# Kernel tuning notes

Measured on AMD Instinct MI355X. Metric: run time of the kernel, lower is better.

## Reference

```python
import jax, jax.numpy as jnp
import numpy as np

N_HEAD = 16
N_EMBD = 1024
HEAD_DIM = N_EMBD // N_HEAD
ROPE_BASE = 10000.0


def _rope_tables(T, dim):
    inv_freq = 1.0 / (ROPE_BASE ** (jnp.arange(0, dim, 2, dtype=jnp.float32) / dim))
    t = jnp.arange(T, dtype=jnp.float32)
    freqs = jnp.einsum('i,j->ij', t, inv_freq)          # [T, dim/2]
    emb = jnp.concatenate((freqs, freqs), axis=-1)       # [T, dim]
    return jnp.cos(emb), jnp.sin(emb)


def _rotate_half(x):
    x1, x2 = jnp.split(x, 2, axis=-1)
    return jnp.concatenate((-x2, x1), axis=-1)


def setup_inputs() -> dict:
    key = jax.random.key(0)
    k_x, k_wa, k_ba, k_wp, k_bp = jax.random.split(key, 5)
    B, T, C = 2, 2048, N_EMBD
    x = jax.random.normal(k_x, (B, T, C), dtype=jnp.float32)
    # torch Linear weights: [out, in]
    W_attn = jax.random.normal(k_wa, (3 * C, C), dtype=jnp.float32) * (1.0 / np.sqrt(C))
    b_attn = jax.random.normal(k_ba, (3 * C,), dtype=jnp.float32) * 0.01
    W_proj = jax.random.normal(k_wp, (C, C), dtype=jnp.float32) * (1.0 / np.sqrt(C))
    b_proj = jax.random.normal(k_bp, (C,), dtype=jnp.float32) * 0.01
    return {"x": x, "W_attn": W_attn, "b_attn": b_attn, "W_proj": W_proj, "b_proj": b_proj}


def reference(x, W_attn, b_attn, W_proj, b_proj):
    B, T, C = x.shape
    H, D = N_HEAD, HEAD_DIM
    qkv = jnp.einsum('btc,oc->bto', x, W_attn) + b_attn   # [B,T,3C]
    q, k, v = jnp.split(qkv, 3, axis=2)
    # [B,T,C] -> [B,H,T,D]
    q = q.reshape(B, T, H, D).transpose(0, 2, 1, 3)
    k = k.reshape(B, T, H, D).transpose(0, 2, 1, 3)
    v = v.reshape(B, T, H, D).transpose(0, 2, 1, 3)
    cos, sin = _rope_tables(T, D)                          # [T,D]
    q = q * cos + _rotate_half(q) * sin
    k = k * cos + _rotate_half(k) * sin
    att = jnp.einsum('bhqd,bhkd->bhqk', q, k) * (1.0 / np.sqrt(D))
    causal = jnp.tril(jnp.ones((T, T), dtype=bool))
    att = jnp.where(causal, att, -jnp.inf)
    att = jax.nn.softmax(att, axis=-1)
    y = jnp.einsum('bhqk,bhkd->bhqd', att, v)              # [B,H,T,D]
    y = y.transpose(0, 2, 1, 3).reshape(B, T, C)
    y = jnp.einsum('btc,oc->bto', y, W_proj) + b_proj
    return y
```

## Files before the change

kernel.cpp:

```cpp
#include <hip/hip_runtime.h>


typedef unsigned short u16;
typedef u16 u16x4 __attribute__((ext_vector_type(4)));
typedef u16 u16x8 __attribute__((ext_vector_type(8)));
typedef short s16x4 __attribute__((ext_vector_type(4)));
typedef short s16x8 __attribute__((ext_vector_type(8)));
typedef float f32x4 __attribute__((ext_vector_type(4)));

#define T_SEQ 2048
#define C_EMB 1024
#define NH 16
#define HD 64

#define MFMA16(a, b, c) __builtin_amdgcn_mfma_f32_16x16x32_bf16(a, b, c, 0, 0, 0)

__device__ __forceinline__ f32x4 MFMA16K16(s16x4 a, s16x4 b, f32x4 c) {
#if __has_builtin(__builtin_amdgcn_mfma_f32_16x16x16bf16_1k)
    return __builtin_amdgcn_mfma_f32_16x16x16bf16_1k(a, b, c, 0, 0, 0);
#else
    asm("v_mfma_f32_16x16x16_bf16 %0, %1, %2, %0" : "+v"(c) : "v"(a), "v"(b));
    return c;
#endif
}

__device__ __forceinline__ u16 f2bf(float f) {
    union { float f; unsigned int i; } x; x.f = f;
    unsigned int r = x.i + 0x7fffu + ((x.i >> 16) & 1u);
    return (u16)(r >> 16);
}
__device__ __forceinline__ u16x4 pack4(f32x4 v) {
    u16x4 o;
#pragma unroll
    for (int j = 0; j < 4; ++j) o[j] = f2bf(v[j]);
    return o;
}
__device__ __forceinline__ s16x4 pack4cvt_s(f32x4 v) {
    union { s16x4 h; unsigned int w[2]; } u;
    asm("v_cvt_pk_bf16_f32 %0, %1, %2" : "=v"(u.w[0]) : "v"(v[0]), "v"(v[1]));
    asm("v_cvt_pk_bf16_f32 %0, %1, %2" : "=v"(u.w[1]) : "v"(v[2]), "v"(v[3]));
    return u.h;
}
__device__ __forceinline__ void gload16(const void* g, void* l) {
    __builtin_amdgcn_global_load_lds(
        (const __attribute__((address_space(1))) unsigned int*)g,
        (__attribute__((address_space(3))) unsigned int*)l, 16, 0, 0);
}

__global__ __launch_bounds__(256) void prep_k(const float* __restrict__ x, const float* __restrict__ Wa,
                                              const float* __restrict__ Wp,
                                              u16* __restrict__ xb, u16* __restrict__ Wab,
                                              u16* __restrict__ Wpb, float2* __restrict__ tab) {
    int bid = blockIdx.x, tid = threadIdx.x;
    if (bid < 4096) {
        const float* src;
        u16* dst;
        int i;
        if (bid < 2048)      { src = x;  dst = xb;  i = bid * 256 + tid; }
        else if (bid < 3584) { src = Wa; dst = Wab; i = (bid - 2048) * 256 + tid; }
        else                 { src = Wp; dst = Wpb; i = (bid - 3584) * 256 + tid; }
        f32x4 a = ((const f32x4*)src)[i * 2];
        f32x4 b = ((const f32x4*)src)[i * 2 + 1];
        u16x8 o;
#pragma unroll
        for (int j = 0; j < 4; ++j) o[j] = f2bf(a[j]);
#pragma unroll
        for (int j = 0; j < 4; ++j) o[4 + j] = f2bf(b[j]);
        ((u16x8*)dst)[i] = o;
    } else {
        int idx = (bid - 4096) * 256 + tid;
        int t = idx >> 5, j = idx & 31;
        float inv = __builtin_exp2f(-0.41524101186092f * (float)j);
        float s_, c_;
        sincosf((float)t * inv, &s_, &c_);
        tab[idx] = make_float2(c_, s_);
    }
}

__global__ __launch_bounds__(256) void qkv_rope_k(const u16* __restrict__ xb, const u16* __restrict__ Wab,
                                                  const float* __restrict__ bias,
                                                  const float2* __restrict__ tab,
                                                  u16* __restrict__ qb, u16* __restrict__ kb,
                                                  u16* __restrict__ vt) {
    __shared__ u16 smem[17408];
    u16* As = smem;
    u16* Bs = smem + 8192;
    int tid = threadIdx.x;
    int n0 = blockIdx.x * 128, m0 = blockIdx.y * 128;
    int w = tid >> 6, lane = tid & 63, lr = lane & 15, quad = lane >> 4;
    int wr = w >> 1, wc = w & 1;
    f32x4 acc[4][4] = {};
    int srow = tid >> 2;
    int swc8 = (((tid & 3) ^ (srow & 3)) << 3);
    int soff = tid * 8;
    int rc8 = ((quad ^ (lr & 3)) << 3);

#define QKV_STAGE(bufi, kc) do {                                                   \
        int _b = (bufi) * 4096;                                                    \
        gload16(xb  + (size_t)(m0 + srow) * C_EMB + (kc) + swc8,      &As[_b + soff]);        \
        gload16(xb  + (size_t)(m0 + 64 + srow) * C_EMB + (kc) + swc8, &As[_b + 2048 + soff]); \
        gload16(Wab + (size_t)(n0 + srow) * C_EMB + (kc) + swc8,      &Bs[_b + soff]);        \
        gload16(Wab + (size_t)(n0 + 64 + srow) * C_EMB + (kc) + swc8, &Bs[_b + 2048 + soff]); \
    } while (0)

    QKV_STAGE(0, 0);
#pragma unroll 2
    for (int kt = 0; kt < 32; ++kt) {
        int cur = kt & 1;
        if (kt < 31) {
            QKV_STAGE(cur ^ 1, (kt + 1) * 32);
            asm volatile("s_waitcnt vmcnt(4)" ::: "memory");
        } else {
            asm volatile("s_waitcnt vmcnt(0)" ::: "memory");
        }
        __builtin_amdgcn_s_barrier();
        asm volatile("" ::: "memory");
        int cb = cur * 4096;
        s16x8 af[4], bf[4];
#pragma unroll
        for (int i = 0; i < 4; ++i)
            af[i] = *(const s16x8*)&As[cb + (wr * 64 + i * 16 + lr) * 32 + rc8];
#pragma unroll
        for (int j = 0; j < 4; ++j)
            bf[j] = *(const s16x8*)&Bs[cb + (wc * 64 + j * 16 + lr) * 32 + rc8];
#pragma unroll
        for (int i = 0; i < 4; ++i)
#pragma unroll
            for (int j = 0; j < 4; ++j) acc[i][j] = MFMA16(af[i], bf[j], acc[i][j]);
        asm volatile("" ::: "memory");
        __builtin_amdgcn_s_barrier();
    }
#undef QKV_STAGE

    int sec = n0 >> 10;
    float bv[4];
#pragma unroll
    for (int j = 0; j < 4; ++j) bv[j] = bias[n0 + wc * 64 + j * 16 + lr];

    int h0 = (n0 & 1023) >> 6;
    int b = m0 >> 11, tbase = m0 & 2047;
    if (sec == 2) {
        u16* Ct = smem;
#pragma unroll
        for (int i = 0; i < 4; ++i)
#pragma unroll
            for (int j = 0; j < 4; ++j) {
                f32x4 vv;
#pragma unroll
                for (int r = 0; r < 4; ++r) vv[r] = acc[i][j][r] + bv[j];
                int d = wc * 64 + j * 16 + lr;
                int m4 = wr * 64 + i * 16 + quad * 4;
                *(u16x4*)&Ct[d * 136 + m4] = pack4(vv);
            }
        __syncthreads();
        size_t hb = (size_t)(b * NH);
#pragma unroll
        for (int p = 0; p < 8; ++p) {
            int idx = p * 256 + tid;
            int d = idx >> 4, mc = (idx & 15) << 3;
            s16x8 vdat = *(const s16x8*)&Ct[d * 136 + mc];
            int h = h0 + (d >> 6), dd = d & 63;
            *(s16x8*)(vt + ((hb + h) * HD + dd) * T_SEQ + tbase + mc) = vdat;
        }
    } else {
        u16* dst = (sec == 0) ? qb : kb;
        float qs = (sec == 0) ? 0.18033688011112043f : 1.0f;
        u16* Ct = smem;
        __syncthreads();
#pragma unroll
        for (int i = 0; i < 4; ++i)
#pragma unroll
            for (int r = 0; r < 4; ++r) {
                int mrow = wr * 64 + i * 16 + quad * 4 + r;
                int t = (m0 + mrow) & 2047;
#pragma unroll
                for (int j = 0; j < 2; ++j) {
                    int d1 = j * 16 + lr;
                    float2 cs = tab[t * 32 + d1];
                    float v1 = acc[i][j][r] + bv[j];
                    float v2 = acc[i][j + 2][r] + bv[j + 2];
                    int n1 = wc * 64 + j * 16 + lr;
                    Ct[mrow * 136 + n1]      = f2bf((v1 * cs.x - v2 * cs.y) * qs);
                    Ct[mrow * 136 + n1 + 32] = f2bf((v2 * cs.x + v1 * cs.y) * qs);
                }
            }
        __syncthreads();
#pragma unroll
        for (int p = 0; p < 8; ++p) {
            int idx = p * 256 + tid;
            int mrow = idx >> 4, c = idx & 15;
            s16x8 vdat = *(const s16x8*)&Ct[mrow * 136 + c * 8];
            int h = h0 + (c >> 3), dd = (c & 7) << 3;
            *(s16x8*)(dst + ((size_t)(b * NH + h) * T_SEQ + tbase + mrow) * HD + dd) = vdat;
        }
    }
}

__global__ __launch_bounds__(512, 4) void flash_k(const u16* __restrict__ qb, const u16* __restrict__ kb,
                                                  const u16* __restrict__ vt, u16* __restrict__ yab) {
    __shared__ u16 Ks[2][64 * 72];
    __shared__ u16 Vs[2][64 * 72];
    int tid = threadIdx.x;
    int bx = blockIdx.x, by = blockIdx.y;
    int qt = (by < 16) ? (15 - bx) : bx;
    int bh = by;
    int w = tid >> 6, lane = tid & 63, lr = lane & 15, quad = lane >> 4;
    int q0 = qt * 128;
    const u16* qh = qb + (size_t)bh * T_SEQ * HD;
    const u16* kh = kb + (size_t)bh * T_SEQ * HD;
    const u16* vh = vt + (size_t)bh * HD * T_SEQ;

    int rbase = q0 + w * 16;

    s16x8 aq[2];
#pragma unroll
    for (int ks = 0; ks < 2; ++ks)
        aq[ks] = *(const s16x8*)(qh + (size_t)(rbase + lr) * HD + ks * 32 + quad * 8);

    int srow = tid >> 3, sc8 = (tid & 7) << 3;

    float m_i = -1e30f;
    f32x4 l4 = {0.f, 0.f, 0.f, 0.f};
    f32x4 oacc[4] = {};

    int ktmax = 2 * qt + 1;
    {
        s16x8 kr0 = *(const s16x8*)(kh + (size_t)srow * HD + sc8);
        s16x8 vr0 = *(const s16x8*)(vh + (size_t)srow * T_SEQ + sc8);
        *(s16x8*)&Ks[0][srow * 72 + sc8] = kr0;
        *(s16x8*)&Vs[0][srow * 72 + sc8] = vr0;
    }
    __syncthreads();

    for (int kt = 0; kt <= ktmax; ++kt) {
        int cur = kt & 1;
        int k0 = kt * 64;
        bool pf = kt < ktmax;
        s16x8 kr0, vr0;
        if (pf) {
            int kn = k0 + 64;
            kr0 = *(const s16x8*)(kh + (size_t)(kn + srow) * HD + sc8);
            vr0 = *(const s16x8*)(vh + (size_t)srow * T_SEQ + kn + sc8);
        }
        const u16* Kc = Ks[cur];
        const u16* Vc = Vs[cur];

        if (k0 <= rbase + 15) {
            s16x8 ak[2][4];
#pragma unroll
            for (int ks = 0; ks < 2; ++ks)
#pragma unroll
                for (int tc = 0; tc < 4; ++tc)
                    ak[ks][tc] = *(const s16x8*)&Kc[(tc * 16 + lr) * 72 + ks * 32 + quad * 8];
            f32x4 sacc[4] = {};
#pragma unroll
            for (int ks = 0; ks < 2; ++ks)
#pragma unroll
                for (int tc = 0; tc < 4; ++tc) sacc[tc] = MFMA16(ak[ks][tc], aq[ks], sacc[tc]);
            if (k0 + 63 > rbase) {
#pragma unroll
                for (int tc = 0; tc < 4; ++tc)
#pragma unroll
                    for (int r = 0; r < 4; ++r)
                        if (k0 + tc * 16 + quad * 4 + r > rbase + lr) sacc[tc][r] = -1e30f;
            }
            f32x4 mv = sacc[0];
#pragma unroll
            for (int tc = 1; tc < 4; ++tc)
#pragma unroll
                for (int r = 0; r < 4; ++r) mv[r] = fmaxf(mv[r], sacc[tc][r]);
            float loc = fmaxf(fmaxf(mv[0], mv[1]), fmaxf(mv[2], mv[3]));
            bool need = !__all(loc <= m_i + 8.0f);
            float alpha = 1.0f;
            if (need) {
                float mx = fmaxf(loc, __shfl_xor(loc, 16, 64));
                mx = fmaxf(mx, __shfl_xor(mx, 32, 64));
                float mn = fmaxf(m_i, mx);
                alpha = __builtin_exp2f(m_i - mn);
                m_i = mn;
#pragma unroll
                for (int r = 0; r < 4; ++r) l4[r] *= alpha;
            }
            float mnow = m_i;
#pragma unroll
            for (int tc = 0; tc < 4; ++tc)
#pragma unroll
                for (int r = 0; r < 4; ++r) {
                    float p = __builtin_exp2f(sacc[tc][r] - mnow);
                    sacc[tc][r] = p;
                    l4[r] += p;
                }
            s16x4 pa[4];
#pragma unroll
            for (int tc = 0; tc < 4; ++tc) pa[tc] = pack4cvt_s(sacc[tc]);
            if (need) {
#pragma unroll
                for (int dn = 0; dn < 4; ++dn)
#pragma unroll
                    for (int r = 0; r < 4; ++r) oacc[dn][r] *= alpha;
            }
#pragma unroll
            for (int dn = 0; dn < 4; ++dn) {
                const u16* vrow = &Vc[(dn * 16 + lr) * 72 + quad * 4];
#pragma unroll
                for (int tc = 0; tc < 4; ++tc) {
                    s16x4 vv = *(const s16x4*)(vrow + tc * 16);
                    oacc[dn] = MFMA16K16(vv, pa[tc], oacc[dn]);
                }
            }
        }
        if (pf) {
            int nx = cur ^ 1;
            *(s16x8*)&Ks[nx][srow * 72 + sc8] = kr0;
            *(s16x8*)&Vs[nx][srow * 72 + sc8] = vr0;
        }
        __syncthreads();
    }
    float rs = (l4[0] + l4[1]) + (l4[2] + l4[3]);
    rs += __shfl_xor(rs, 16, 64);
    rs += __shfl_xor(rs, 32, 64);
    int b = bh >> 4, hh = bh & 15;
    {
        float inv = 1.f / rs;
        int t = rbase + lr;
        size_t base = ((size_t)b * T_SEQ + t) * C_EMB + hh * HD;
#pragma unroll
        for (int dn = 0; dn < 4; ++dn) {
            f32x4 vv;
#pragma unroll
            for (int r = 0; r < 4; ++r) vv[r] = oacc[dn][r] * inv;
            *(u16x4*)(yab + base + dn * 16 + quad * 4) = pack4(vv);
        }
    }
}

__global__ __launch_bounds__(256) void proj_k(const u16* __restrict__ ya, const u16* __restrict__ Wpb,
                                              const float* __restrict__ bias, float* __restrict__ out) {
    __shared__ u16 As[2][2048];
    __shared__ u16 Bs[2][2048];
    int tid = threadIdx.x;
    int n0 = blockIdx.x * 64, m0 = blockIdx.y * 64;
    int w = tid >> 6, lane = tid & 63, lr = lane & 15, quad = lane >> 4;
    int wr = w >> 1, wc = w & 1;
    f32x4 acc[2][2] = {};
    int srow = tid >> 2;
    int swc8 = (((tid & 3) ^ (srow & 3)) << 3);
    int soff = tid * 8;
    int rc8 = ((quad ^ (lr & 3)) << 3);

#define PRJ_STAGE(bufi, kc) do {                                                   \
        gload16(ya  + (size_t)(m0 + srow) * C_EMB + (kc) + swc8, &As[bufi][soff]); \
        gload16(Wpb + (size_t)(n0 + srow) * C_EMB + (kc) + swc8, &Bs[bufi][soff]); \
    } while (0)

    PRJ_STAGE(0, 0);
#pragma unroll 2
    for (int kt = 0; kt < 32; ++kt) {
        int cur = kt & 1;
        if (kt < 31) {
            PRJ_STAGE(cur ^ 1, (kt + 1) * 32);
            asm volatile("s_waitcnt vmcnt(2)" ::: "memory");
        } else {
            asm volatile("s_waitcnt vmcnt(0)" ::: "memory");
        }
        __builtin_amdgcn_s_barrier();
        asm volatile("" ::: "memory");
        s16x8 af[2], bf[2];
#pragma unroll
        for (int i = 0; i < 2; ++i)
            af[i] = *(const s16x8*)&As[cur][(wr * 32 + i * 16 + lr) * 32 + rc8];
#pragma unroll
        for (int j = 0; j < 2; ++j)
            bf[j] = *(const s16x8*)&Bs[cur][(wc * 32 + j * 16 + lr) * 32 + rc8];
#pragma unroll
        for (int i = 0; i < 2; ++i)
#pragma unroll
            for (int j = 0; j < 2; ++j) acc[i][j] = MFMA16(af[i], bf[j], acc[i][j]);
        asm volatile("" ::: "memory");
        __builtin_amdgcn_s_barrier();
    }
#undef PRJ_STAGE

    float bv[2];
#pragma unroll
    for (int j = 0; j < 2; ++j) bv[j] = bias[n0 + wc * 32 + j * 16 + lr];
#pragma unroll
    for (int i = 0; i < 2; ++i)
#pragma unroll
        for (int r = 0; r < 4; ++r) {
            int m = m0 + wr * 32 + i * 16 + quad * 4 + r;
#pragma unroll
            for (int j = 0; j < 2; ++j)
                out[(size_t)m * C_EMB + n0 + wc * 32 + j * 16 + lr] = acc[i][j][r] + bv[j];
        }
}

extern "C" void kernel_launch(void* const* d_in, const int* in_sizes, int n_in,
                              void* d_out, int out_size, void* d_ws, size_t ws_size,
                              hipStream_t stream) {
    const float *x = nullptr, *Wa = nullptr, *ba = nullptr, *Wp = nullptr, *bp = nullptr;
    for (int i = 0; i < n_in; ++i) {
        switch (in_sizes[i]) {
            case 4194304: x  = (const float*)d_in[i]; break;
            case 3145728: Wa = (const float*)d_in[i]; break;
            case 3072:    ba = (const float*)d_in[i]; break;
            case 1048576: Wp = (const float*)d_in[i]; break;
            case 1024:    bp = (const float*)d_in[i]; break;
            default: break;
        }
    }
    float* out = (float*)d_out;

    char* ws = (char*)d_ws;
    u16* qb     = (u16*)(ws);
    u16* kb     = (u16*)(ws + 8388608);
    u16* vt     = (u16*)(ws + 16777216);
    u16* yab    = (u16*)(ws + 25165824);
    float2* tab = (float2*)(ws + 33554432);
    u16* xb     = (u16*)(ws + 35651584);
    u16* Wab    = (u16*)(ws + 44040192);
    u16* Wpb    = (u16*)(ws + 50331648);

    prep_k<<<4352, 256, 0, stream>>>(x, Wa, Wp, xb, Wab, Wpb, tab);
    qkv_rope_k<<<dim3(24, 32), 256, 0, stream>>>(xb, Wab, ba, tab, qb, kb, vt);
    flash_k<<<dim3(16, 32), 512, 0, stream>>>(qb, kb, vt, yab);
    proj_k<<<dim3(16, 64), 256, 0, stream>>>(yab, Wpb, bp, out);
}
```

Before: 195.0 us.

## Process two query strips per wave in flash attention to reuse K/V fragments

The flash kernel now runs with 256 threads (4 waves), and each wave handles two 16-row query strips. The strips are paired so that strip w goes with strip 7-w, which balances causal work across waves. K and V fragments are read from shared memory once per tile and used for both strips, which halves LDS traffic per unit of work and evens out the causal load within a block. The cost is more registers per thread (two sets of accumulators and softmax state) and fewer waves per block, which could reduce latency hiding.

```diff
diff --git a/kernel.cpp b/kernel.cpp
--- a/kernel.cpp
+++ b/kernel.cpp
@@ -196,7 +196,7 @@
     }
 }
 
-__global__ __launch_bounds__(512, 4) void flash_k(const u16* __restrict__ qb, const u16* __restrict__ kb,
+__global__ __launch_bounds__(256, 2) void flash_k(const u16* __restrict__ qb, const u16* __restrict__ kb,
                                                   const u16* __restrict__ vt, u16* __restrict__ yab) {
     __shared__ u16 Ks[2][64 * 72];
     __shared__ u16 Vs[2][64 * 72];
@@ -210,25 +210,33 @@
     const u16* kh = kb + (size_t)bh * T_SEQ * HD;
     const u16* vh = vt + (size_t)bh * HD * T_SEQ;
 
-    int rbase = q0 + w * 16;
-
-    s16x8 aq[2];
-#pragma unroll
-    for (int ks = 0; ks < 2; ++ks)
-        aq[ks] = *(const s16x8*)(qh + (size_t)(rbase + lr) * HD + ks * 32 + quad * 8);
+    int rb[2];
+    rb[0] = q0 + w * 16;
+    rb[1] = q0 + 112 - w * 16;
+
+    s16x8 aq[2][2];
+#pragma unroll
+    for (int s = 0; s < 2; ++s)
+#pragma unroll
+        for (int ks = 0; ks < 2; ++ks)
+            aq[s][ks] = *(const s16x8*)(qh + (size_t)(rb[s] + lr) * HD + ks * 32 + quad * 8);
 
     int srow = tid >> 3, sc8 = (tid & 7) << 3;
 
-    float m_i = -1e30f;
-    f32x4 l4 = {0.f, 0.f, 0.f, 0.f};
-    f32x4 oacc[4] = {};
+    float m_i[2] = {-1e30f, -1e30f};
+    f32x4 l4[2] = {{0.f, 0.f, 0.f, 0.f}, {0.f, 0.f, 0.f, 0.f}};
+    f32x4 oacc[2][4] = {};
 
     int ktmax = 2 * qt + 1;
     {
-        s16x8 kr0 = *(const s16x8*)(kh + (size_t)srow * HD + sc8);
-        s16x8 vr0 = *(const s16x8*)(vh + (size_t)srow * T_SEQ + sc8);
-        *(s16x8*)&Ks[0][srow * 72 + sc8] = kr0;
-        *(s16x8*)&Vs[0][srow * 72 + sc8] = vr0;
+        s16x8 ka = *(const s16x8*)(kh + (size_t)srow * HD + sc8);
+        s16x8 kb2 = *(const s16x8*)(kh + (size_t)(srow + 32) * HD + sc8);
+        s16x8 va = *(const s16x8*)(vh + (size_t)srow * T_SEQ + sc8);
+        s16x8 vb = *(const s16x8*)(vh + (size_t)(srow + 32) * T_SEQ + sc8);
+        *(s16x8*)&Ks[0][srow * 72 + sc8] = ka;
+        *(s16x8*)&Ks[0][(srow + 32) * 72 + sc8] = kb2;
+        *(s16x8*)&Vs[0][srow * 72 + sc8] = va;
+        *(s16x8*)&Vs[0][(srow + 32) * 72 + sc8] = vb;
     }
     __syncthreads();
 
@@ -236,99 +244,113 @@
         int cur = kt & 1;
         int k0 = kt * 64;
         bool pf = kt < ktmax;
-        s16x8 kr0, vr0;
+        s16x8 kr0, kr1, vr0, vr1;
         if (pf) {
             int kn = k0 + 64;
             kr0 = *(const s16x8*)(kh + (size_t)(kn + srow) * HD + sc8);
+            kr1 = *(const s16x8*)(kh + (size_t)(kn + srow + 32) * HD + sc8);
             vr0 = *(const s16x8*)(vh + (size_t)srow * T_SEQ + kn + sc8);
+            vr1 = *(const s16x8*)(vh + (size_t)(srow + 32) * T_SEQ + kn + sc8);
         }
         const u16* Kc = Ks[cur];
         const u16* Vc = Vs[cur];
 
-        if (k0 <= rbase + 15) {
+        if (k0 <= rb[1] + 15) {
             s16x8 ak[2][4];
 #pragma unroll
             for (int ks = 0; ks < 2; ++ks)
 #pragma unroll
                 for (int tc = 0; tc < 4; ++tc)
                     ak[ks][tc] = *(const s16x8*)&Kc[(tc * 16 + lr) * 72 + ks * 32 + quad * 8];
-            f32x4 sacc[4] = {};
-#pragma unroll
-            for (int ks = 0; ks < 2; ++ks)
-#pragma unroll
-                for (int tc = 0; tc < 4; ++tc) sacc[tc] = MFMA16(ak[ks][tc], aq[ks], sacc[tc]);
-            if (k0 + 63 > rbase) {
-#pragma unroll
-                for (int tc = 0; tc < 4; ++tc)
-#pragma unroll
-                    for (int r = 0; r < 4; ++r)
-                        if (k0 + tc * 16 + quad * 4 + r > rbase + lr) sacc[tc][r] = -1e30f;
-            }
-            f32x4 mv = sacc[0];
-#pragma unroll
-            for (int tc = 1; tc < 4; ++tc)
-#pragma unroll
-                for (int r = 0; r < 4; ++r) mv[r] = fmaxf(mv[r], sacc[tc][r]);
-            float loc = fmaxf(fmaxf(mv[0], mv[1]), fmaxf(mv[2], mv[3]));
-            bool need = !__all(loc <= m_i + 8.0f);
-            float alpha = 1.0f;
-            if (need) {
-                float mx = fmaxf(loc, __shfl_xor(loc, 16, 64));
-                mx = fmaxf(mx, __shfl_xor(mx, 32, 64));
-                float mn = fmaxf(m_i, mx);
-                alpha = __builtin_exp2f(m_i - mn);
-                m_i = mn;
-#pragma unroll
-                for (int r = 0; r < 4; ++r) l4[r] *= alpha;
-            }
-            float mnow = m_i;
-#pragma unroll
-            for (int tc = 0; tc < 4; ++tc)
-#pragma unroll
-                for (int r = 0; r < 4; ++r) {
-                    float p = __builtin_exp2f(sacc[tc][r] - mnow);
-                    sacc[tc][r] = p;
-                    l4[r] += p;
-                }
-            s16x4 pa[4];
-#pragma unroll
-            for (int tc = 0; tc < 4; ++tc) pa[tc] = pack4cvt_s(sacc[tc]);
-            if (need) {
-#pragma unroll
-                for (int dn = 0; dn < 4; ++dn)
-#pragma unroll
-                    for (int r = 0; r < 4; ++r) oacc[dn][r] *= alpha;
-            }
+            s16x4 av[4][4];
 #pragma unroll
             for (int dn = 0; dn < 4; ++dn) {
                 const u16* vrow = &Vc[(dn * 16 + lr) * 72 + quad * 4];
 #pragma unroll
-                for (int tc = 0; tc < 4; ++tc) {
-                    s16x4 vv = *(const s16x4*)(vrow + tc * 16);
-                    oacc[dn] = MFMA16K16(vv, pa[tc], oacc[dn]);
+                for (int tc = 0; tc < 4; ++tc)
+                    av[dn][tc] = *(const s16x4*)(vrow + tc * 16);
+            }
+#pragma unroll
+            for (int s = 0; s < 2; ++s) {
+                int rbase = rb[s];
+                if (k0 > rbase + 15) continue;
+                f32x4 sacc[4] = {};
+#pragma unroll
+                for (int ks = 0; ks < 2; ++ks)
+#pragma unroll
+                    for (int tc = 0; tc < 4; ++tc) sacc[tc] = MFMA16(ak[ks][tc], aq[s][ks], sacc[tc]);
+                if (k0 + 63 > rbase) {
+#pragma unroll
+                    for (int tc = 0; tc < 4; ++tc)
+#pragma unroll
+                        for (int r = 0; r < 4; ++r)
+                            if (k0 + tc * 16 + quad * 4 + r > rbase + lr) sacc[tc][r] = -1e30f;
                 }
+                f32x4 mv = sacc[0];
+#pragma unroll
+                for (int tc = 1; tc < 4; ++tc)
+#pragma unroll
+                    for (int r = 0; r < 4; ++r) mv[r] = fmaxf(mv[r], sacc[tc][r]);
+                float loc = fmaxf(fmaxf(mv[0], mv[1]), fmaxf(mv[2], mv[3]));
+                bool need = !__all(loc <= m_i[s] + 8.0f);
+                float alpha = 1.0f;
+                if (need) {
+                    float mx = fmaxf(loc, __shfl_xor(loc, 16, 64));
+                    mx = fmaxf(mx, __shfl_xor(mx, 32, 64));
+                    float mn = fmaxf(m_i[s], mx);
+                    alpha = __builtin_exp2f(m_i[s] - mn);
+                    m_i[s] = mn;
+#pragma unroll
+                    for (int r = 0; r < 4; ++r) l4[s][r] *= alpha;
+                }
+                float mnow = m_i[s];
+#pragma unroll
+                for (int tc = 0; tc < 4; ++tc)
+#pragma unroll
+                    for (int r = 0; r < 4; ++r) {
+                        float p = __builtin_exp2f(sacc[tc][r] - mnow);
+                        sacc[tc][r] = p;
+                        l4[s][r] += p;
+                    }
+                s16x4 pa[4];
+#pragma unroll
+                for (int tc = 0; tc < 4; ++tc) pa[tc] = pack4cvt_s(sacc[tc]);
+                if (need) {
+#pragma unroll
+                    for (int dn = 0; dn < 4; ++dn)
+#pragma unroll
+                        for (int r = 0; r < 4; ++r) oacc[s][dn][r] *= alpha;
+                }
+#pragma unroll
+                for (int dn = 0; dn < 4; ++dn)
+#pragma unroll
+                    for (int tc = 0; tc < 4; ++tc)
+                        oacc[s][dn] = MFMA16K16(av[dn][tc], pa[tc], oacc[s][dn]);
             }
         }
         if (pf) {
             int nx = cur ^ 1;
             *(s16x8*)&Ks[nx][srow * 72 + sc8] = kr0;
+            *(s16x8*)&Ks[nx][(srow + 32) * 72 + sc8] = kr1;
             *(s16x8*)&Vs[nx][srow * 72 + sc8] = vr0;
+            *(s16x8*)&Vs[nx][(srow + 32) * 72 + sc8] = vr1;
         }
         __syncthreads();
     }
-    float rs = (l4[0] + l4[1]) + (l4[2] + l4[3]);
-    rs += __shfl_xor(rs, 16, 64);
-    rs += __shfl_xor(rs, 32, 64);
     int b = bh >> 4, hh = bh & 15;
-    {
+#pragma unroll
+    for (int s = 0; s < 2; ++s) {
+        float rs = (l4[s][0] + l4[s][1]) + (l4[s][2] + l4[s][3]);
+        rs += __shfl_xor(rs, 16, 64);
+        rs += __shfl_xor(rs, 32, 64);
         float inv = 1.f / rs;
-        int t = rbase + lr;
+        int t = rb[s] + lr;
         size_t base = ((size_t)b * T_SEQ + t) * C_EMB + hh * HD;
 #pragma unroll
         for (int dn = 0; dn < 4; ++dn) {
             f32x4 vv;
 #pragma unroll
-            for (int r = 0; r < 4; ++r) vv[r] = oacc[dn][r] * inv;
+            for (int r = 0; r < 4; ++r) vv[r] = oacc[s][dn][r] * inv;
             *(u16x4*)(yab + base + dn * 16 + quad * 4) = pack4(vv);
         }
     }
@@ -423,6 +445,6 @@
 
     prep_k<<<4352, 256, 0, stream>>>(x, Wa, Wp, xb, Wab, Wpb, tab);
     qkv_rope_k<<<dim3(24, 32), 256, 0, stream>>>(xb, Wab, ba, tab, qb, kb, vt);
-    flash_k<<<dim3(16, 32), 512, 0, stream>>>(qb, kb, vt, yab);
+    flash_k<<<dim3(16, 32), 256, 0, stream>>>(qb, kb, vt, yab);
     proj_k<<<dim3(16, 64), 256, 0, stream>>>(yab, Wpb, bp, out);
 }
```

Result: slower. 200.3 us (+2.7%).

## Triple-buffer QKV GEMM loads and shrink flash attention tiles to 64 queries

Applied to the files above, without the earlier changes.

The QKV projection GEMM moves from double to triple buffering in shared memory, so global loads are issued two k-steps ahead with adjusted vmcnt waits. The flash attention kernel changes from 512-thread blocks with 128-query tiles to 256-thread blocks with 64-query tiles. This doubles the grid, removes the per-wave skip branch since every wave now needs every key tile up to the diagonal, and applies the causal mask only on the last tile. V fragments are also loaded into registers before the QK MFMAs. The aim is to hide memory latency and improve load balance across the causal triangle, at the cost of more LDS in the GEMM and more register pressure in attention.

```diff
diff --git a/kernel.cpp b/kernel.cpp
--- a/kernel.cpp
+++ b/kernel.cpp
@@ -82,9 +82,9 @@
                                                   const float2* __restrict__ tab,
                                                   u16* __restrict__ qb, u16* __restrict__ kb,
                                                   u16* __restrict__ vt) {
-    __shared__ u16 smem[17408];
+    __shared__ u16 smem[24576];
     u16* As = smem;
-    u16* Bs = smem + 8192;
+    u16* Bs = smem + 12288;
     int tid = threadIdx.x;
     int n0 = blockIdx.x * 128, m0 = blockIdx.y * 128;
     int w = tid >> 6, lane = tid & 63, lr = lane & 15, quad = lane >> 4;
@@ -104,11 +104,14 @@
     } while (0)
 
     QKV_STAGE(0, 0);
-#pragma unroll 2
+    QKV_STAGE(1, 32);
+    int cur = 0;
     for (int kt = 0; kt < 32; ++kt) {
-        int cur = kt & 1;
-        if (kt < 31) {
-            QKV_STAGE(cur ^ 1, (kt + 1) * 32);
+        if (kt < 30) {
+            int nb = cur + 2; if (nb >= 3) nb -= 3;
+            QKV_STAGE(nb, (kt + 2) * 32);
+            asm volatile("s_waitcnt vmcnt(8)" ::: "memory");
+        } else if (kt == 30) {
             asm volatile("s_waitcnt vmcnt(4)" ::: "memory");
         } else {
             asm volatile("s_waitcnt vmcnt(0)" ::: "memory");
@@ -129,6 +132,7 @@
             for (int j = 0; j < 4; ++j) acc[i][j] = MFMA16(af[i], bf[j], acc[i][j]);
         asm volatile("" ::: "memory");
         __builtin_amdgcn_s_barrier();
+        cur = cur + 1; if (cur >= 3) cur -= 3;
     }
 #undef QKV_STAGE
 
@@ -196,16 +200,16 @@
     }
 }
 
-__global__ __launch_bounds__(512, 4) void flash_k(const u16* __restrict__ qb, const u16* __restrict__ kb,
+__global__ __launch_bounds__(256, 4) void flash_k(const u16* __restrict__ qb, const u16* __restrict__ kb,
                                                   const u16* __restrict__ vt, u16* __restrict__ yab) {
     __shared__ u16 Ks[2][64 * 72];
     __shared__ u16 Vs[2][64 * 72];
     int tid = threadIdx.x;
     int bx = blockIdx.x, by = blockIdx.y;
-    int qt = (by < 16) ? (15 - bx) : bx;
+    int qt = (by < 16) ? (31 - bx) : bx;
     int bh = by;
     int w = tid >> 6, lane = tid & 63, lr = lane & 15, quad = lane >> 4;
-    int q0 = qt * 128;
+    int q0 = qt * 64;
     const u16* qh = qb + (size_t)bh * T_SEQ * HD;
     const u16* kh = kb + (size_t)bh * T_SEQ * HD;
     const u16* vh = vt + (size_t)bh * HD * T_SEQ;
@@ -223,12 +227,16 @@
     f32x4 l4 = {0.f, 0.f, 0.f, 0.f};
     f32x4 oacc[4] = {};
 
-    int ktmax = 2 * qt + 1;
+    int ktmax = qt;
     {
-        s16x8 kr0 = *(const s16x8*)(kh + (size_t)srow * HD + sc8);
-        s16x8 vr0 = *(const s16x8*)(vh + (size_t)srow * T_SEQ + sc8);
-        *(s16x8*)&Ks[0][srow * 72 + sc8] = kr0;
-        *(s16x8*)&Vs[0][srow * 72 + sc8] = vr0;
+        s16x8 ka = *(const s16x8*)(kh + (size_t)srow * HD + sc8);
+        s16x8 kb2 = *(const s16x8*)(kh + (size_t)(srow + 32) * HD + sc8);
+        s16x8 va = *(const s16x8*)(vh + (size_t)srow * T_SEQ + sc8);
+        s16x8 vb = *(const s16x8*)(vh + (size_t)(srow + 32) * T_SEQ + sc8);
+        *(s16x8*)&Ks[0][srow * 72 + sc8] = ka;
+        *(s16x8*)&Ks[0][(srow + 32) * 72 + sc8] = kb2;
+        *(s16x8*)&Vs[0][srow * 72 + sc8] = va;
+        *(s16x8*)&Vs[0][(srow + 32) * 72 + sc8] = vb;
     }
     __syncthreads();
 
@@ -236,83 +244,90 @@
         int cur = kt & 1;
         int k0 = kt * 64;
         bool pf = kt < ktmax;
-        s16x8 kr0, vr0;
+        s16x8 kr0, kr1, vr0, vr1;
         if (pf) {
             int kn = k0 + 64;
             kr0 = *(const s16x8*)(kh + (size_t)(kn + srow) * HD + sc8);
+            kr1 = *(const s16x8*)(kh + (size_t)(kn + srow + 32) * HD + sc8);
             vr0 = *(const s16x8*)(vh + (size_t)srow * T_SEQ + kn + sc8);
+            vr1 = *(const s16x8*)(vh + (size_t)(srow + 32) * T_SEQ + kn + sc8);
         }
         const u16* Kc = Ks[cur];
         const u16* Vc = Vs[cur];
 
-        if (k0 <= rbase + 15) {
-            s16x8 ak[2][4];
-#pragma unroll
-            for (int ks = 0; ks < 2; ++ks)
-#pragma unroll
-                for (int tc = 0; tc < 4; ++tc)
-                    ak[ks][tc] = *(const s16x8*)&Kc[(tc * 16 + lr) * 72 + ks * 32 + quad * 8];
-            f32x4 sacc[4] = {};
-#pragma unroll
-            for (int ks = 0; ks < 2; ++ks)
-#pragma unroll
-                for (int tc = 0; tc < 4; ++tc) sacc[tc] = MFMA16(ak[ks][tc], aq[ks], sacc[tc]);
-            if (k0 + 63 > rbase) {
-#pragma unroll
-                for (int tc = 0; tc < 4; ++tc)
-#pragma unroll
-                    for (int r = 0; r < 4; ++r)
-                        if (k0 + tc * 16 + quad * 4 + r > rbase + lr) sacc[tc][r] = -1e30f;
+        s16x8 ak[2][4];
+#pragma unroll
+        for (int ks = 0; ks < 2; ++ks)
+#pragma unroll
+            for (int tc = 0; tc < 4; ++tc)
+                ak[ks][tc] = *(const s16x8*)&Kc[(tc * 16 + lr) * 72 + ks * 32 + quad * 8];
+        s16x4 av[4][4];
+#pragma unroll
+        for (int dn = 0; dn < 4; ++dn) {
+            const u16* vrow = &Vc[(dn * 16 + lr) * 72 + quad * 4];
+#pragma unroll
+            for (int tc = 0; tc < 4; ++tc)
+                av[dn][tc] = *(const s16x4*)(vrow + tc * 16);
+        }
+        f32x4 sacc[4] = {};
+#pragma unroll
+        for (int ks = 0; ks < 2; ++ks)
+#pragma unroll
+            for (int tc = 0; tc < 4; ++tc) sacc[tc] = MFMA16(ak[ks][tc], aq[ks], sacc[tc]);
+        if (kt == ktmax) {
+#pragma unroll
+            for (int tc = 0; tc < 4; ++tc)
+#pragma unroll
+                for (int r = 0; r < 4; ++r)
+                    if (k0 + tc * 16 + quad * 4 + r > rbase + lr) sacc[tc][r] = -1e30f;
+        }
+        f32x4 mv = sacc[0];
+#pragma unroll
+        for (int tc = 1; tc < 4; ++tc)
+#pragma unroll
+            for (int r = 0; r < 4; ++r) mv[r] = fmaxf(mv[r], sacc[tc][r]);
+        float loc = fmaxf(fmaxf(mv[0], mv[1]), fmaxf(mv[2], mv[3]));
+        bool need = !__all(loc <= m_i + 8.0f);
+        float alpha = 1.0f;
+        if (need) {
+            float mx = fmaxf(loc, __shfl_xor(loc, 16, 64));
+            mx = fmaxf(mx, __shfl_xor(mx, 32, 64));
+            float mn = fmaxf(m_i, mx);
+            alpha = __builtin_exp2f(m_i - mn);
+            m_i = mn;
+#pragma unroll
+            for (int r = 0; r < 4; ++r) l4[r] *= alpha;
+        }
+        float mnow = m_i;
+#pragma unroll
+        for (int tc = 0; tc < 4; ++tc)
+#pragma unroll
+            for (int r = 0; r < 4; ++r) {
+                float p = __builtin_exp2f(sacc[tc][r] - mnow);
+                sacc[tc][r] = p;
+                l4[r] += p;
             }
-            f32x4 mv = sacc[0];
-#pragma unroll
-            for (int tc = 1; tc < 4; ++tc)
-#pragma unroll
-                for (int r = 0; r < 4; ++r) mv[r] = fmaxf(mv[r], sacc[tc][r]);
-            float loc = fmaxf(fmaxf(mv[0], mv[1]), fmaxf(mv[2], mv[3]));
-            bool need = !__all(loc <= m_i + 8.0f);
-            float alpha = 1.0f;
-            if (need) {
-                float mx = fmaxf(loc, __shfl_xor(loc, 16, 64));
-                mx = fmaxf(mx, __shfl_xor(mx, 32, 64));
-                float mn = fmaxf(m_i, mx);
-                alpha = __builtin_exp2f(m_i - mn);
-                m_i = mn;
-#pragma unroll
-                for (int r = 0; r < 4; ++r) l4[r] *= alpha;
-            }
-            float mnow = m_i;
+        s16x4 pa[4];
+#pragma unroll
+        for (int tc = 0; tc < 4; ++tc) pa[tc] = pack4cvt_s(sacc[tc]);
+        if (need) {
+#pragma unroll
+            for (int dn = 0; dn < 4; ++dn)
+#pragma unroll
+                for (int r = 0; r < 4; ++r) oacc[dn][r] *= alpha;
+        }
+#pragma unroll
+        for (int dn = 0; dn < 4; ++dn)
 #pragma unroll
             for (int tc = 0; tc < 4; ++tc)
-#pragma unroll
-                for (int r = 0; r < 4; ++r) {
-                    float p = __builtin_exp2f(sacc[tc][r] - mnow);
-                    sacc[tc][r] = p;
-                    l4[r] += p;
-                }
-            s16x4 pa[4];
-#pragma unroll
-            for (int tc = 0; tc < 4; ++tc) pa[tc] = pack4cvt_s(sacc[tc]);
-            if (need) {
-#pragma unroll
-                for (int dn = 0; dn < 4; ++dn)
-#pragma unroll
-                    for (int r = 0; r < 4; ++r) oacc[dn][r] *= alpha;
-            }
-#pragma unroll
-            for (int dn = 0; dn < 4; ++dn) {
-                const u16* vrow = &Vc[(dn * 16 + lr) * 72 + quad * 4];
-#pragma unroll
-                for (int tc = 0; tc < 4; ++tc) {
-                    s16x4 vv = *(const s16x4*)(vrow + tc * 16);
-                    oacc[dn] = MFMA16K16(vv, pa[tc], oacc[dn]);
-                }
-            }
-        }
+                oacc[dn] = MFMA16K16(av[dn][tc], pa[tc], oacc[dn]);
+
         if (pf) {
             int nx = cur ^ 1;
             *(s16x8*)&Ks[nx][srow * 72 + sc8] = kr0;
+            *(s16x8*)&Ks[nx][(srow + 32) * 72 + sc8] = kr1;
             *(s16x8*)&Vs[nx][srow * 72 + sc8] = vr0;
+            *(s16x8*)&Vs[nx][(srow + 32) * 72 + sc8] = vr1;
         }
         __syncthreads();
     }
@@ -423,6 +438,6 @@
 
     prep_k<<<4352, 256, 0, stream>>>(x, Wa, Wp, xb, Wab, Wpb, tab);
     qkv_rope_k<<<dim3(24, 32), 256, 0, stream>>>(xb, Wab, ba, tab, qb, kb, vt);
-    flash_k<<<dim3(16, 32), 512, 0, stream>>>(qb, kb, vt, yab);
+    flash_k<<<dim3(32, 32), 256, 0, stream>>>(qb, kb, vt, yab);
     proj_k<<<dim3(16, 64), 256, 0, stream>>>(yab, Wpb, bp, out);
 }
```

After: 190.4 us. 2.4% less time.
